# Kernel optimization log

Measured on AMD Instinct MI355X. Metric: run time of the kernel, lower is better.

## Reference

```python
import jax, jax.numpy as jnp
import numpy as np

N = 50000          # num_nodes
IN_CH = 128
H = 32             # hidden_channels
D = 2              # stalk dimension d (= final_d, add_lp=add_hp=False)
LAYERS = 4
EU = 400000        # undirected edges
E = 2 * EU         # directed edges (both orientations)
OUT = 32


def setup_inputs() -> dict:
    key = jax.random.key(0)
    ks = jax.random.split(key, 12)
    # undirected random graph; directed edge list holds both orientations so that
    # the reverse of directed edge e is e + EU (mod E)
    u = jax.random.randint(ks[0], (EU,), 0, N)
    v = jax.random.randint(ks[1], (EU,), 0, N)
    edge_index = jnp.stack([jnp.concatenate([u, v]), jnp.concatenate([v, u])]).astype(jnp.int64)
    x = jax.random.normal(ks[2], (N, IN_CH), dtype=jnp.float32)
    W1 = jax.random.normal(ks[3], (H * D, IN_CH), dtype=jnp.float32) / np.sqrt(IN_CH)
    b1 = jax.random.normal(ks[4], (H * D,), dtype=jnp.float32) * 0.01
    W_sheaf = jax.random.normal(ks[5], (LAYERS, D, 2 * D * H), dtype=jnp.float32) / np.sqrt(2 * D * H)
    # lin_left initialised to identity in the module; keep near-identity
    W_left = jnp.tile(jnp.eye(D, dtype=jnp.float32), (LAYERS, 1, 1)) \
        + 0.01 * jax.random.normal(ks[6], (LAYERS, D, D), dtype=jnp.float32)
    W_right = jax.random.normal(ks[7], (LAYERS, H, H), dtype=jnp.float32) / np.sqrt(H)
    eps = jnp.zeros((LAYERS, D, 1), dtype=jnp.float32) + 0.01 * jax.random.normal(ks[8], (LAYERS, D, 1), dtype=jnp.float32)
    W2 = jax.random.normal(ks[9], (OUT, D * H), dtype=jnp.float32) / np.sqrt(D * H)
    b2 = jax.random.normal(ks[10], (OUT,), dtype=jnp.float32) * 0.01
    return {"x": x, "edge_index": edge_index, "W1": W1, "b1": b1, "W_sheaf": W_sheaf,
            "W_left": W_left, "W_right": W_right, "eps": eps, "W2": W2, "b2": b2}


def reference(x, edge_index, W1, b1, W_sheaf, W_left, W_right, eps, W2, b2):
    # eval mode: dropouts are no-ops; diagnostic energies/eigsh omitted (no effect on output)
    n = x.shape[0]
    d = W_left.shape[-1]
    h = W_right.shape[-1]
    src, dst = edge_index[0], edge_index[1]
    e = src.shape[0]
    rev = (jnp.arange(e) + e // 2) % e  # reverse directed edge

    x = jax.nn.elu(x @ W1.T + b1)      # [N, d*h]
    x = x.reshape(n * d, h)
    x0 = x

    for l in range(W_left.shape[0]):
        # --- sheaf learner: tanh(Linear([x_i || x_j])), diag maps F: [E, d] ---
        xn = x.reshape(n, d * h)
        feat = jnp.concatenate([xn[src], xn[dst]], axis=-1)   # [E, 2dh]
        F = jnp.tanh(feat @ W_sheaf[l].T)                     # [E, d]
        Fr = F[rev]
        # --- diag sheaf Laplacian (normalised, augmented: D_hat = D + I) ---
        Dg = jax.ops.segment_sum(F * F, src, num_segments=n)  # [N, d] diagonal blocks
        dinv = jax.lax.rsqrt(Dg + 1.0)
        diagw = Dg * dinv * dinv                              # [N, d]
        offw = -F * Fr * dinv[src] * dinv[dst]                # [E, d]
        # --- left weights: view x^T as [h, N, d], mix stalk dim ---
        xt = x.T.reshape(h, n, d) @ W_left[l].T
        x = xt.reshape(h, n * d).T
        # --- right weights ---
        x = x @ W_right[l].T
        # --- spmm: y = L x ---
        x3 = x.reshape(n, d, h)
        y = diagw[:, :, None] * x3 \
            + jax.ops.segment_sum(offw[:, :, None] * x3[dst], src, num_segments=n)
        x = jax.nn.elu(y.reshape(n * d, h))
        # --- epsilon-gated residual ---
        coeff = jnp.tile(1.0 + jnp.tanh(eps[l]), (n, 1))      # [N*d, 1]
        x0 = coeff * x0 - x
        x = x0

    return x.reshape(n, d * h) @ W2.T + b2
```

## Files before the change

### kernel.cpp

```cpp
#include <hip/hip_runtime.h>
#include <math.h>

#define INCH 128
#define DH 64
#define H  32
#define D  2
#define LAYERS 4
#define OUTC 32

typedef __fp16 half2h __attribute__((ext_vector_type(2)));
typedef __fp16 half4 __attribute__((ext_vector_type(4)));
typedef __fp16 half8 __attribute__((ext_vector_type(8)));
typedef float  f32x4 __attribute__((ext_vector_type(4)));

__device__ __forceinline__ float eluf(float v) { return v > 0.f ? v : expm1f(v); }

__device__ __forceinline__ float ftanh(float x) {
    float xc = fminf(9.0f, fmaxf(-9.0f, x));
    float e2 = __builtin_amdgcn_exp2f(xc * 2.885390081777927f);
    return (e2 - 1.0f) * __builtin_amdgcn_rcpf(e2 + 1.0f);
}

__global__ void k_prep(const float* __restrict__ W1, const float* __restrict__ W2,
                       const float* __restrict__ Wleft, const float* __restrict__ Wright,
                       __fp16* __restrict__ W1h, __fp16* __restrict__ W2h,
                       __fp16* __restrict__ Mlrh) {
    int idx = blockIdx.x * blockDim.x + threadIdx.x;
    if (idx < DH * INCH) {
        W1h[idx] = (__fp16)W1[idx];
    } else if (idx < DH * INCH + OUTC * DH) {
        int i = idx - DH * INCH;
        W2h[i] = (__fp16)W2[i];
    } else if (idx < DH * INCH + OUTC * DH + LAYERS * DH * DH) {
        int i = idx - DH * INCH - OUTC * DH;
        int l = i >> 12;
        int r = i & 4095;
        int row = r >> 6;
        int col = r & 63;
        int sp = row >> 5, c = row & 31;
        int s  = col >> 5, cp = col & 31;
        Mlrh[i] = (__fp16)(Wleft[l * 4 + sp * 2 + s] * Wright[l * 1024 + c * 32 + cp]);
    }
}

__global__ void k_hist(const int* __restrict__ src, int* __restrict__ deg, int E) {
    int e = blockIdx.x * blockDim.x + threadIdx.x;
    if (e < E) atomicAdd(&deg[src[e]], 1);
}

__global__ void k_bsum(const int* __restrict__ deg, int* __restrict__ bsum, int N) {
    int b = blockIdx.x, t = threadIdx.x;
    int lane = t & 63, wid = t >> 6;
    int base = b * 1024 + t * 4;
    int s = 0;
    #pragma unroll
    for (int i = 0; i < 4; ++i) {
        int idx = base + i;
        if (idx < N) s += deg[idx];
    }
    #pragma unroll
    for (int ofs = 32; ofs; ofs >>= 1) s += __shfl_xor(s, ofs);
    __shared__ int ws[4];
    if (lane == 0) ws[wid] = s;
    __syncthreads();
    if (t == 0) bsum[b] = ws[0] + ws[1] + ws[2] + ws[3];
}

__global__ void k_scan_small(int* __restrict__ bsum, int B) {
    int lane = threadIdx.x;
    int carry = 0;
    for (int base = 0; base < B; base += 64) {
        int i = base + lane;
        int v = (i < B) ? bsum[i] : 0;
        int incl = v;
        #pragma unroll
        for (int ofs = 1; ofs < 64; ofs <<= 1) {
            int tt = __shfl_up(incl, ofs);
            if (lane >= ofs) incl += tt;
        }
        if (i < B) bsum[i] = carry + incl - v;
        carry += __shfl(incl, 63);
    }
}

__global__ void k_scan_final(const int* __restrict__ deg, const int* __restrict__ bsum,
                             int* __restrict__ rowptr, int* __restrict__ cur, int N) {
    int b = blockIdx.x, t = threadIdx.x;
    int lane = t & 63, wid = t >> 6;
    int base = b * 1024 + t * 4;
    int v[4];
    int s = 0;
    #pragma unroll
    for (int i = 0; i < 4; ++i) {
        int idx = base + i;
        v[i] = (idx < N) ? deg[idx] : 0;
        s += v[i];
    }
    int incl = s;
    #pragma unroll
    for (int ofs = 1; ofs < 64; ofs <<= 1) {
        int tt = __shfl_up(incl, ofs);
        if (lane >= ofs) incl += tt;
    }
    __shared__ int ws[4];
    if (lane == 63) ws[wid] = incl;
    __syncthreads();
    int woff = 0;
    for (int k = 0; k < wid; ++k) woff += ws[k];
    int excl = bsum[b] + woff + incl - s;
    #pragma unroll
    for (int i = 0; i < 4; ++i) {
        int idx = base + i;
        if (idx < N) { rowptr[idx] = excl; cur[idx] = excl; }
        excl += v[i];
        if (idx == N - 1) rowptr[N] = excl;
    }
}

__global__ void k_scatter(const int* __restrict__ src, const int* __restrict__ dst,
                          int* __restrict__ cur, unsigned short* __restrict__ csr_dst, int E) {
    int e = blockIdx.x * blockDim.x + threadIdx.x;
    if (e >= E) return;
    int pos = atomicAdd(&cur[src[e]], 1);
    csr_dst[pos] = (unsigned short)dst[e];
}


__global__ __launch_bounds__(256) void k_mlp1_pq(const float* __restrict__ xin,
                                                 const __fp16* __restrict__ W1h,
                                                 const float* __restrict__ b1,
                                                 const float* __restrict__ Ws0,
                                                 float* __restrict__ X,
                                                 __fp16* __restrict__ NDh, int N) {
    __shared__ float xs[16 * INCH];
    __shared__ __fp16 wsh[DH * 132];
    __shared__ float xout[16 * DH];
    int t = threadIdx.x;
    int node0 = blockIdx.x * 16;
    for (int i = t; i < 16 * INCH / 4; i += 256) {
        int r = i >> 5, c = (i & 31) * 4;
        int node = node0 + r;
        f32x4 v = (node < N) ? __builtin_nontemporal_load((const f32x4*)(xin + (size_t)node * INCH + c))
                             : (f32x4){0.f, 0.f, 0.f, 0.f};
        *(f32x4*)&xs[r * INCH + c] = v;
    }
    for (int i = t; i < DH * INCH / 4; i += 256) {
        int r = i >> 5, c = (i & 31) * 4;
        *(uint2*)&wsh[r * 132 + c] = ((const uint2*)W1h)[i];
    }
    __syncthreads();
    int w = t >> 6, lane = t & 63;
    int oc0 = w * 16;
    int rr = lane & 15, g = lane >> 4;
    f32x4 acc = {0.f, 0.f, 0.f, 0.f};
    #pragma unroll
    for (int ks = 0; ks < INCH / 16; ++ks) {
        f32x4 xv = *(const f32x4*)&xs[rr * INCH + ks * 16 + g * 4];
        half4 af = {(__fp16)xv.x, (__fp16)xv.y, (__fp16)xv.z, (__fp16)xv.w};
        half4 bf = *(const half4*)&wsh[(oc0 + rr) * 132 + ks * 16 + g * 4];
        acc = __builtin_amdgcn_mfma_f32_16x16x16f16(af, bf, acc, 0, 0, 0);
    }
    int oc = oc0 + rr;
    float bb = b1[oc];
    #pragma unroll
    for (int r = 0; r < 4; ++r) {
        int node = node0 + g * 4 + r;
        float v = eluf(acc[r] + bb);
        xout[(g * 4 + r) * DH + oc] = v;
        if (node < N) X[(size_t)node * DH + oc] = v;
    }
    __syncthreads();
    float wsa = Ws0[lane];
    float wsb = Ws0[64 + lane];
    float wsc = Ws0[128 + lane];
    float wsd = Ws0[192 + lane];
    #pragma unroll
    for (int j = 0; j < 4; ++j) {
        int nl = w * 4 + j;
        int node = node0 + nl;
        float x = xout[nl * DH + lane];
        float p0 = x * wsa, q0 = x * wsb, p1 = x * wsc, q1 = x * wsd;
        #pragma unroll
        for (int ofs = 32; ofs; ofs >>= 1) {
            p0 += __shfl_xor(p0, ofs);
            q0 += __shfl_xor(q0, ofs);
            p1 += __shfl_xor(p1, ofs);
            q1 += __shfl_xor(q1, ofs);
        }
        if (lane == 0 && node < N) {
            half4 pq = {(__fp16)p0, (__fp16)p1, (__fp16)q0, (__fp16)q1};
            *(half4*)(NDh + (size_t)node * 8) = pq;
        }
    }
}

__global__ __launch_bounds__(256) void k_dglr(__fp16* __restrict__ NDh,
                                              const int* __restrict__ rowptr,
                                              const unsigned short* __restrict__ csr_dst,
                                              const float* __restrict__ X,
                                              const __fp16* __restrict__ Mlrh_l,
                                              __fp16* __restrict__ XWI,
                                              int Bdg, int N) {
    __shared__ float xs[16 * DH];
    __shared__ __fp16 mlh[DH * 68];
    if (blockIdx.x < Bdg) {
        int lane = threadIdx.x & 63;
        int widl = threadIdx.x >> 6;
        int nn = lane >> 4, sub = lane & 15;
        int node = blockIdx.x * 16 + widl * 4 + nn;
        if (node >= N) return;
        half4 pqu = *(const half4*)(NDh + (size_t)node * 8);
        float pu0 = (float)pqu[0], pu1 = (float)pqu[1];
        int pos = rowptr[node], end = rowptr[node + 1];
        float sx = 0.f, sy = 0.f;
        for (int i = pos + sub; i < end; i += 16) {
            int v = (int)__builtin_nontemporal_load(csr_dst + i);
            half4 pqv = *(const half4*)(NDh + (size_t)v * 8);
            float fx = ftanh(pu0 + (float)pqv[2]);
            float fy = ftanh(pu1 + (float)pqv[3]);
            sx += fx * fx;
            sy += fy * fy;
        }
        #pragma unroll
        for (int ofs = 8; ofs; ofs >>= 1) {
            sx += __shfl_xor(sx, ofs);
            sy += __shfl_xor(sy, ofs);
        }
        if (sub == 0) {
            float i0 = 1.f / (sx + 1.f), i1 = 1.f / (sy + 1.f);
            half4 gi = {(__fp16)sqrtf(i0), (__fp16)sqrtf(i1), (__fp16)(sx * i0), (__fp16)(sy * i1)};
            *(half4*)(NDh + (size_t)node * 8 + 4) = gi;
        }
        return;
    }
    int t = threadIdx.x;
    int node0 = (blockIdx.x - Bdg) * 16;
    for (int i = t; i < 16 * DH / 4; i += 256) {
        int r = i >> 4, c = (i & 15) * 4;
        int node = node0 + r;
        f32x4 v = (node < N) ? __builtin_nontemporal_load((const f32x4*)(X + (size_t)node * DH + c))
                             : (f32x4){0.f, 0.f, 0.f, 0.f};
        *(f32x4*)&xs[r * DH + c] = v;
    }
    for (int i = t; i < DH * DH / 4; i += 256) {
        int r = i >> 4, c = (i & 15) * 4;
        *(uint2*)&mlh[r * 68 + c] = ((const uint2*)Mlrh_l)[i];
    }
    __syncthreads();
    int w = t >> 6, lane = t & 63;
    int oc0 = w * 16;
    int rr = lane & 15, g = lane >> 4;
    f32x4 acc = {0.f, 0.f, 0.f, 0.f};
    #pragma unroll
    for (int ks = 0; ks < DH / 16; ++ks) {
        f32x4 xv = *(const f32x4*)&xs[rr * DH + ks * 16 + g * 4];
        half4 af = {(__fp16)xv.x, (__fp16)xv.y, (__fp16)xv.z, (__fp16)xv.w};
        half4 bf = *(const half4*)&mlh[(oc0 + rr) * 68 + ks * 16 + g * 4];
        acc = __builtin_amdgcn_mfma_f32_16x16x16f16(af, bf, acc, 0, 0, 0);
    }
    int oc = oc0 + rr;
    int sp = oc >> 5, c = oc & 31;
    int cidx = (c >> 2) * 8 + sp * 4 + (c & 3);
    #pragma unroll
    for (int r = 0; r < 4; ++r) {
        int node = node0 + g * 4 + r;
        if (node < N) XWI[(size_t)node * 64 + cidx] = (__fp16)acc[r];
    }
}

__global__ __launch_bounds__(256) void k_out(const float* __restrict__ X,
                                             const __fp16* __restrict__ W2h,
                                             const float* __restrict__ b2,
                                             float* __restrict__ out, int N) {
    __shared__ float xs[32 * DH];
    __shared__ __fp16 w2s[OUTC * 68];
    int t = threadIdx.x;
    int node0 = blockIdx.x * 32;
    for (int i = t; i < 32 * DH / 4; i += 256) {
        int r = i >> 4, c = (i & 15) * 4;
        int node = node0 + r;
        f32x4 v = (node < N) ? __builtin_nontemporal_load((const f32x4*)(X + (size_t)node * DH + c))
                             : (f32x4){0.f, 0.f, 0.f, 0.f};
        *(f32x4*)&xs[r * DH + c] = v;
    }
    for (int i = t; i < OUTC * DH / 4; i += 256) {
        int r = i >> 4, c = (i & 15) * 4;
        *(uint2*)&w2s[r * 68 + c] = ((const uint2*)W2h)[i];
    }
    __syncthreads();
    int w = t >> 6, lane = t & 63;
    int nt = w >> 1;
    int oc0 = (w & 1) * 16;
    int rr = lane & 15, g = lane >> 4;
    f32x4 acc = {0.f, 0.f, 0.f, 0.f};
    #pragma unroll
    for (int ks = 0; ks < DH / 16; ++ks) {
        f32x4 xv = *(const f32x4*)&xs[(nt * 16 + rr) * DH + ks * 16 + g * 4];
        half4 af = {(__fp16)xv.x, (__fp16)xv.y, (__fp16)xv.z, (__fp16)xv.w};
        half4 bf = *(const half4*)&w2s[(oc0 + rr) * 68 + ks * 16 + g * 4];
        acc = __builtin_amdgcn_mfma_f32_16x16x16f16(af, bf, acc, 0, 0, 0);
    }
    int oc = oc0 + rr;
    float bb = b2[oc];
    #pragma unroll
    for (int r = 0; r < 4; ++r) {
        int node = node0 + nt * 16 + g * 4 + r;
        if (node < N) out[(size_t)node * OUTC + oc] = acc[r] + bb;
    }
}

__global__ void k_spmm_fin_pq(const __fp16* __restrict__ XWI,
                              const __fp16* __restrict__ NDh, const int* __restrict__ rowptr,
                              const unsigned short* __restrict__ csr_dst,
                              const float* __restrict__ eps_l, const float* __restrict__ Wsn,
                              float* __restrict__ X, __fp16* __restrict__ NDhn, int N) {
    int wid = (blockIdx.x * blockDim.x + threadIdx.x) >> 6;
    int lane = threadIdx.x & 63;
    if (wid >= N) return;
    int q = lane >> 3;
    int m = lane & 7;
    half8 ndu = *(const half8*)(NDh + (size_t)wid * 8);
    float pu0 = (float)ndu[0], pu1 = (float)ndu[1];
    float qu0 = (float)ndu[2], qu1 = (float)ndu[3];
    float dinv0 = (float)ndu[4], dinv1 = (float)ndu[5];
    int pos = rowptr[wid], end = rowptr[wid + 1];

    float a0x = 0.f, a0y = 0.f, a0z = 0.f, a0w = 0.f;
    float a1x = 0.f, a1y = 0.f, a1z = 0.f, a1w = 0.f;

    for (int chunk = pos; chunk < end; chunk += 64) {
        int myidx = chunk + lane;
        int dmy = 0;
        unsigned wpkmy = 0;
        if (myidx < end) {
            dmy = (int)__builtin_nontemporal_load(csr_dst + myidx);
            half8 ndd = *(const half8*)(NDh + (size_t)dmy * 8);
            float ff0 = ftanh(pu0 + (float)ndd[2]), fb0 = ftanh((float)ndd[0] + qu0);
            float ff1 = ftanh(pu1 + (float)ndd[3]), fb1 = ftanh((float)ndd[1] + qu1);
            float w0 = -ff0 * fb0 * dinv0 * (float)ndd[4];
            float w1 = -ff1 * fb1 * dinv1 * (float)ndd[5];
            half2h wp = {(__fp16)w0, (__fp16)w1};
            __builtin_memcpy(&wpkmy, &wp, 4);
        }
        int lim = end - chunk; if (lim > 64) lim = 64;
        for (int b = 0; b < lim; b += 8) {
            int sl = b + q;
            int d        = __shfl(dmy, sl);
            unsigned wpk = __shfl((int)wpkmy, sl);
            half2h wp;
            __builtin_memcpy(&wp, &wpk, 4);
            float w0e = (float)wp.x, w1e = (float)wp.y;
            half8 g = *(const half8*)(XWI + (size_t)d * 64 + m * 8);
            a0x += w0e * (float)g[0]; a0y += w0e * (float)g[1];
            a0z += w0e * (float)g[2]; a0w += w0e * (float)g[3];
            a1x += w1e * (float)g[4]; a1y += w1e * (float)g[5];
            a1z += w1e * (float)g[6]; a1w += w1e * (float)g[7];
        }
    }
    #pragma unroll
    for (int ofs = 8; ofs <= 32; ofs <<= 1) {
        a0x += __shfl_xor(a0x, ofs); a0y += __shfl_xor(a0y, ofs);
        a0z += __shfl_xor(a0z, ofs); a0w += __shfl_xor(a0w, ofs);
        a1x += __shfl_xor(a1x, ofs); a1y += __shfl_xor(a1y, ofs);
        a1z += __shfl_xor(a1z, ofs); a1w += __shfl_xor(a1w, ofs);
    }
    if (q == 0) {
        float diag0 = (float)ndu[6];
        float diag1 = (float)ndu[7];
        half8 xw = *(const half8*)(XWI + (size_t)wid * 64 + m * 8);
        size_t b0 = (size_t)wid * DH + m * 4;
        size_t b1 = b0 + 32;
        float coeff0 = 1.f + tanhf(eps_l[0]);
        float coeff1 = 1.f + tanhf(eps_l[1]);
        f32x4 xo0 = __builtin_nontemporal_load((const f32x4*)(X + b0));
        f32x4 xo1 = __builtin_nontemporal_load((const f32x4*)(X + b1));
        f32x4 xn0, xn1;
        xn0.x = coeff0 * xo0.x - eluf(diag0 * (float)xw[0] + a0x);
        xn0.y = coeff0 * xo0.y - eluf(diag0 * (float)xw[1] + a0y);
        xn0.z = coeff0 * xo0.z - eluf(diag0 * (float)xw[2] + a0z);
        xn0.w = coeff0 * xo0.w - eluf(diag0 * (float)xw[3] + a0w);
        xn1.x = coeff1 * xo1.x - eluf(diag1 * (float)xw[4] + a1x);
        xn1.y = coeff1 * xo1.y - eluf(diag1 * (float)xw[5] + a1y);
        xn1.z = coeff1 * xo1.z - eluf(diag1 * (float)xw[6] + a1z);
        xn1.w = coeff1 * xo1.w - eluf(diag1 * (float)xw[7] + a1w);
        __builtin_nontemporal_store(xn0, (f32x4*)(X + b0));
        __builtin_nontemporal_store(xn1, (f32x4*)(X + b1));
        if (Wsn) {
            f32x4 wa0 = *(const f32x4*)(Wsn + m * 4);
            f32x4 wa1 = *(const f32x4*)(Wsn + 32 + m * 4);
            f32x4 wb0 = *(const f32x4*)(Wsn + 64 + m * 4);
            f32x4 wb1 = *(const f32x4*)(Wsn + 96 + m * 4);
            f32x4 wc0 = *(const f32x4*)(Wsn + 128 + m * 4);
            f32x4 wc1 = *(const f32x4*)(Wsn + 160 + m * 4);
            f32x4 wd0 = *(const f32x4*)(Wsn + 192 + m * 4);
            f32x4 wd1 = *(const f32x4*)(Wsn + 224 + m * 4);
            float p0 = xn0.x * wa0.x + xn0.y * wa0.y + xn0.z * wa0.z + xn0.w * wa0.w
                     + xn1.x * wa1.x + xn1.y * wa1.y + xn1.z * wa1.z + xn1.w * wa1.w;
            float q0 = xn0.x * wb0.x + xn0.y * wb0.y + xn0.z * wb0.z + xn0.w * wb0.w
                     + xn1.x * wb1.x + xn1.y * wb1.y + xn1.z * wb1.z + xn1.w * wb1.w;
            float p1 = xn0.x * wc0.x + xn0.y * wc0.y + xn0.z * wc0.z + xn0.w * wc0.w
                     + xn1.x * wc1.x + xn1.y * wc1.y + xn1.z * wc1.z + xn1.w * wc1.w;
            float q1 = xn0.x * wd0.x + xn0.y * wd0.y + xn0.z * wd0.z + xn0.w * wd0.w
                     + xn1.x * wd1.x + xn1.y * wd1.y + xn1.z * wd1.z + xn1.w * wd1.w;
            #pragma unroll
            for (int ofs = 1; ofs < 8; ofs <<= 1) {
                p0 += __shfl_xor(p0, ofs);
                q0 += __shfl_xor(q0, ofs);
                p1 += __shfl_xor(p1, ofs);
                q1 += __shfl_xor(q1, ofs);
            }
            if (m == 0) {
                half4 pq = {(__fp16)p0, (__fp16)p1, (__fp16)q0, (__fp16)q1};
                *(half4*)(NDhn + (size_t)wid * 8) = pq;
            }
        }
    }
}

extern "C" void kernel_launch(void* const* d_in, const int* in_sizes, int n_in,
                              void* d_out, int out_size, void* d_ws, size_t ws_size,
                              hipStream_t stream) {
    const float* xin    = (const float*)d_in[0];
    const int*   ei     = (const int*)d_in[1];
    const float* W1     = (const float*)d_in[2];
    const float* b1     = (const float*)d_in[3];
    const float* Wsheaf = (const float*)d_in[4];
    const float* Wleft  = (const float*)d_in[5];
    const float* Wright = (const float*)d_in[6];
    const float* eps    = (const float*)d_in[7];
    const float* W2     = (const float*)d_in[8];
    const float* b2     = (const float*)d_in[9];
    float* out = (float*)d_out;

    int N = in_sizes[0] / INCH;
    int E = in_sizes[1] / 2;
    const int* src = ei;
    const int* dst = ei + E;

    size_t off = 0;
    auto alloc = [&](size_t nbytes) {
        char* p = (char*)d_ws + off;
        off += (nbytes + 255) & ~(size_t)255;
        return p;
    };
    float*          X       = (float*)alloc((size_t)N * DH * 4);
    __fp16*         XWI     = (__fp16*)alloc((size_t)N * DH * 2);
    __fp16*         NDha    = (__fp16*)alloc((size_t)N * 16);
    __fp16*         NDhb    = (__fp16*)alloc((size_t)N * 16);
    int*            deg     = (int*)alloc((size_t)N * 4);
    int*            rowptr  = (int*)alloc(((size_t)N + 1) * 4);
    int*            cur     = (int*)alloc((size_t)N * 4);
    unsigned short* csr_dst = (unsigned short*)alloc((size_t)E * 2);
    int*            bsum    = (int*)alloc(4096);
    __fp16*         W1h     = (__fp16*)alloc((size_t)DH * INCH * 2);
    __fp16*         W2h     = (__fp16*)alloc((size_t)OUTC * DH * 2);
    __fp16*         Mlrh    = (__fp16*)alloc((size_t)LAYERS * DH * DH * 2);

    int B = (N + 1023) / 1024;

    int prep_total = DH * INCH + OUTC * DH + LAYERS * DH * DH;
    k_prep<<<(prep_total + 255) / 256, 256, 0, stream>>>(W1, W2, Wleft, Wright, W1h, W2h, Mlrh);
    hipMemsetAsync(deg, 0, (size_t)N * sizeof(int), stream);
    k_hist<<<(E + 255) / 256, 256, 0, stream>>>(src, deg, E);
    k_bsum<<<B, 256, 0, stream>>>(deg, bsum, N);
    k_scan_small<<<1, 64, 0, stream>>>(bsum, B);
    k_scan_final<<<B, 256, 0, stream>>>(deg, bsum, rowptr, cur, N);
    k_scatter<<<(E + 255) / 256, 256, 0, stream>>>(src, dst, cur, csr_dst, E);

    k_mlp1_pq<<<(N + 15) / 16, 256, 0, stream>>>(xin, W1h, b1, Wsheaf, X, NDha, N);

    __fp16* NDcur = NDha;
    __fp16* NDnext = NDhb;
    int Bdg = (N + 15) / 16;
    int Blr = (N + 15) / 16;
    for (int l = 0; l < LAYERS; ++l) {
        k_dglr<<<Bdg + Blr, 256, 0, stream>>>(NDcur, rowptr, csr_dst, X,
                                              Mlrh + (size_t)l * DH * DH, XWI, Bdg, N);
        const float* Wsn = (l + 1 < LAYERS) ? (Wsheaf + (l + 1) * 2 * INCH) : nullptr;
        k_spmm_fin_pq<<<(N + 3) / 4, 256, 0, stream>>>(XWI, NDcur, rowptr, csr_dst,
                                                       eps + l * 2, Wsn, X, NDnext, N);
        __fp16* tmp = NDcur; NDcur = NDnext; NDnext = tmp;
    }

    k_out<<<(N + 31) / 32, 256, 0, stream>>>(X, W2h, b2, out, N);
}
```

Measured before the change: 367.7 us.

## Build CSR via two-pass bucketed scatter to localize atomic writes

Replaces the single random-position CSR scatter with a two-pass scheme. Edges are first binned into buckets of 64 source nodes using packed (src,dst) words. A second pass then scatters from the bucketed order, so the per-node atomics and csr_dst writes hit nearby addresses. This aims to cut scattered atomic and write traffic, at the cost of an extra E-sized buffer, an extra histogram atomic per edge, and three more kernel launches.

```diff
diff --git a/kernel.cpp b/kernel.cpp
--- a/kernel.cpp
+++ b/kernel.cpp
@@ -43,9 +43,13 @@
     }
 }
 
-__global__ void k_hist(const int* __restrict__ src, int* __restrict__ deg, int E) {
+__global__ void k_hist(const int* __restrict__ src, int* __restrict__ deg,
+                       int* __restrict__ bcount, int E) {
     int e = blockIdx.x * blockDim.x + threadIdx.x;
-    if (e < E) atomicAdd(&deg[src[e]], 1);
+    if (e >= E) return;
+    int s = src[e];
+    atomicAdd(&deg[s], 1);
+    atomicAdd(&bcount[s >> 6], 1);
 }
 
 __global__ void k_bsum(const int* __restrict__ deg, int* __restrict__ bsum, int N) {
@@ -66,21 +70,26 @@
     if (t == 0) bsum[b] = ws[0] + ws[1] + ws[2] + ws[3];
 }
 
-__global__ void k_scan_small(int* __restrict__ bsum, int B) {
+__global__ void k_scan_small(int* __restrict__ arr, int B) {
     int lane = threadIdx.x;
     int carry = 0;
     for (int base = 0; base < B; base += 64) {
         int i = base + lane;
-        int v = (i < B) ? bsum[i] : 0;
+        int v = (i < B) ? arr[i] : 0;
         int incl = v;
         #pragma unroll
         for (int ofs = 1; ofs < 64; ofs <<= 1) {
             int tt = __shfl_up(incl, ofs);
             if (lane >= ofs) incl += tt;
         }
-        if (i < B) bsum[i] = carry + incl - v;
+        if (i < B) arr[i] = carry + incl - v;
         carry += __shfl(incl, 63);
     }
+}
+
+__global__ void k_copy_int(const int* __restrict__ srcv, int* __restrict__ dstv, int n) {
+    int i = blockIdx.x * blockDim.x + threadIdx.x;
+    if (i < n) dstv[i] = srcv[i];
 }
 
 __global__ void k_scan_final(const int* __restrict__ deg, const int* __restrict__ bsum,
@@ -117,12 +126,23 @@
     }
 }
 
-__global__ void k_scatter(const int* __restrict__ src, const int* __restrict__ dst,
-                          int* __restrict__ cur, unsigned short* __restrict__ csr_dst, int E) {
+__global__ void k_bscatter(const int* __restrict__ src, const int* __restrict__ dst,
+                           int* __restrict__ bcur, unsigned* __restrict__ bedge, int E) {
     int e = blockIdx.x * blockDim.x + threadIdx.x;
     if (e >= E) return;
-    int pos = atomicAdd(&cur[src[e]], 1);
-    csr_dst[pos] = (unsigned short)dst[e];
+    int s = src[e];
+    int p = atomicAdd(&bcur[s >> 6], 1);
+    bedge[p] = ((unsigned)s << 16) | (unsigned)dst[e];
+}
+
+__global__ void k_fscatter(const unsigned* __restrict__ bedge, int* __restrict__ cur,
+                           unsigned short* __restrict__ csr_dst, int E) {
+    int i = blockIdx.x * blockDim.x + threadIdx.x;
+    if (i >= E) return;
+    unsigned pk = bedge[i];
+    int s = (int)(pk >> 16);
+    int p2 = atomicAdd(&cur[s], 1);
+    csr_dst[p2] = (unsigned short)(pk & 0xFFFFu);
 }
 
 
@@ -451,21 +471,29 @@
     int*            rowptr  = (int*)alloc(((size_t)N + 1) * 4);
     int*            cur     = (int*)alloc((size_t)N * 4);
     unsigned short* csr_dst = (unsigned short*)alloc((size_t)E * 2);
+    unsigned*       bedge   = (unsigned*)alloc((size_t)E * 4);
     int*            bsum    = (int*)alloc(4096);
+    int*            bcount  = (int*)alloc(((size_t)(50000 >> 6) + 2) * 4);
+    int*            bcur    = (int*)alloc(((size_t)(50000 >> 6) + 2) * 4);
     __fp16*         W1h     = (__fp16*)alloc((size_t)DH * INCH * 2);
     __fp16*         W2h     = (__fp16*)alloc((size_t)OUTC * DH * 2);
     __fp16*         Mlrh    = (__fp16*)alloc((size_t)LAYERS * DH * DH * 2);
 
     int B = (N + 1023) / 1024;
+    int NB = (N + 63) >> 6;
 
     int prep_total = DH * INCH + OUTC * DH + LAYERS * DH * DH;
     k_prep<<<(prep_total + 255) / 256, 256, 0, stream>>>(W1, W2, Wleft, Wright, W1h, W2h, Mlrh);
     hipMemsetAsync(deg, 0, (size_t)N * sizeof(int), stream);
-    k_hist<<<(E + 255) / 256, 256, 0, stream>>>(src, deg, E);
+    hipMemsetAsync(bcount, 0, (size_t)NB * sizeof(int), stream);
+    k_hist<<<(E + 255) / 256, 256, 0, stream>>>(src, deg, bcount, E);
     k_bsum<<<B, 256, 0, stream>>>(deg, bsum, N);
     k_scan_small<<<1, 64, 0, stream>>>(bsum, B);
+    k_scan_small<<<1, 64, 0, stream>>>(bcount, NB);
+    k_copy_int<<<(NB + 255) / 256, 256, 0, stream>>>(bcount, bcur, NB);
     k_scan_final<<<B, 256, 0, stream>>>(deg, bsum, rowptr, cur, N);
-    k_scatter<<<(E + 255) / 256, 256, 0, stream>>>(src, dst, cur, csr_dst, E);
+    k_bscatter<<<(E + 255) / 256, 256, 0, stream>>>(src, dst, bcur, bedge, E);
+    k_fscatter<<<(E + 255) / 256, 256, 0, stream>>>(bedge, cur, csr_dst, E);
 
     k_mlp1_pq<<<(N + 15) / 16, 256, 0, stream>>>(xin, W1h, b1, Wsheaf, X, NDha, N);
 
```

Measured after the change: 741.5 us. 102% more time.
